# Kernel tuning notes

Hardware: AMD Instinct MI355X
Metric: run time of the kernel (lower is better)

The kernel has to match this reference:

```python
import jax, jax.numpy as jnp
import numpy as np

M, N, D, K = 32, 8192, 64, 16


def setup_inputs() -> dict:
    key = jax.random.key(0)
    ks = jax.random.split(key, 5)
    X = jax.random.normal(ks[0], (N, D), jnp.float32)
    pi = jax.nn.softmax(jax.random.normal(ks[1], (M,), jnp.float32))  # valid mixture weights
    mu = jax.random.normal(ks[2], (M, D), jnp.float32)
    Lambda_j = 0.1 * jax.random.normal(ks[3], (M, D, K), jnp.float32)  # matches .normal_(0, 0.1) init
    Psi = jax.random.uniform(ks[4], (D,), jnp.float32) + 0.1  # positive diagonal noise variances
    return {"X": X, "pi": pi, "mu": mu, "Lambda_j": Lambda_j, "Psi": Psi}


def _e_step(X, pi, mu, Lambda_j, Psi):
    d = X.shape[1]
    k = Lambda_j.shape[2]
    diag_psi = jnp.diag(Psi) + 1e-6 * jnp.eye(d, dtype=X.dtype)
    # Sigma_j = Lambda_j @ Lambda_j^T + diag(Psi), batched over components: [M,D,D]
    Sigma = jnp.einsum('mdk,mek->mde', Lambda_j, Lambda_j) + diag_psi
    chol = jnp.linalg.cholesky(Sigma)  # [M,D,D], same factorization MultivariateNormal uses
    diff = X[None, :, :] - mu[:, None, :]  # [M,N,D]
    # Mahalanobis term via triangular solve: sol = L^{-1} diff^T  -> [M,D,N]
    sol = jax.vmap(lambda L, Dm: jax.scipy.linalg.solve_triangular(L, Dm.T, lower=True))(chol, diff)
    maha = jnp.sum(sol * sol, axis=1)  # [M,N]
    logdet = 2.0 * jnp.sum(jnp.log(jnp.diagonal(chol, axis1=1, axis2=2)), axis=1)  # [M]
    log_prob = -0.5 * (d * jnp.log(2.0 * jnp.pi) + maha) - 0.5 * logdet[:, None]  # [M,N]
    log_h = (jnp.log(pi + 1e-10)[:, None] + log_prob).T  # [N,M]
    responsibilities = jax.nn.softmax(log_h, axis=1)
    # beta_j = Lambda_j^T Sigma_j^{-1}, via Cholesky solve (same math as torch.inverse path)
    SigInvL = jax.vmap(lambda L, Lam: jax.scipy.linalg.cho_solve((L, True), Lam))(chol, Lambda_j)  # [M,D,K]
    beta = jnp.swapaxes(SigInvL, 1, 2)  # [M,K,D]
    e_z = jnp.einsum('mnd,mkd->mnk', diff, beta)  # [M,N,K]
    term1 = jnp.eye(k, dtype=X.dtype) - jnp.einsum('mkd,mdj->mkj', beta, Lambda_j)  # [M,K,K]
    e_zz = term1[:, None, :, :] + jnp.einsum('mni,mnj->mnij', e_z, e_z)  # [M,N,K,K]
    return responsibilities, e_z, e_zz


def reference(X, pi, mu, Lambda_j, Psi):
    return _e_step(X, pi, mu, Lambda_j, Psi)
```

## Files before the change

kernel.cpp:

```cpp
#include <hip/hip_runtime.h>
#include <math.h>

#define MM 32
#define NN 8192
#define DD 64
#define KK 16

__global__ __launch_bounds__(256) void mfa_pre(
    const float* __restrict__ pi, const float* __restrict__ Lambda,
    const float* __restrict__ Psi, float* __restrict__ Minv_out,
    float* __restrict__ const_out) {
  const int m = blockIdx.x;
  const int tid = threadIdx.x;
  __shared__ float lam[DD * KK];
  __shared__ float pinv[DD];
  __shared__ float Mmat[KK * KK];
  __shared__ float Lmat[KK * KK];
  __shared__ float vbuf[KK];

  for (int idx = tid; idx < DD * KK; idx += 256)
    lam[idx] = Lambda[(size_t)m * DD * KK + idx];
  if (tid < DD) pinv[tid] = 1.0f / (Psi[tid] + 1e-6f);
  __syncthreads();

  {
    const int k = tid >> 4, j = tid & 15;
    float a = 0.0f;
    for (int d = 0; d < DD; ++d)
      a += lam[d * KK + k] * lam[d * KK + j] * pinv[d];
    Mmat[tid] = a + (k == j ? 1.0f : 0.0f);
  }
  __syncthreads();

  float lr[KK];
  if (tid < KK) {
#pragma unroll
    for (int j = 0; j < KK; ++j) lr[j] = Mmat[tid * KK + j];
  }
#pragma unroll
  for (int c = 0; c < KK; ++c) {
    if (tid < KK) vbuf[tid] = lr[c];
    __syncthreads();
    if (tid < KK) {
      const float vc = vbuf[c];
      const float dc = sqrtf(vc);
      const float lrc = lr[c] / dc;
      if (tid >= c) Lmat[tid * KK + c] = lrc;
      const float s = lr[c] / vc;
#pragma unroll
      for (int j = 0; j < KK; ++j)
        if (j > c) lr[j] -= s * vbuf[j];
    }
    __syncthreads();
  }

  if (tid < KK) {
    const int col = tid;
    float y[KK], z[KK];
#pragma unroll
    for (int i = 0; i < KK; ++i) {
      float s = (i == col) ? 1.0f : 0.0f;
#pragma unroll
      for (int p = 0; p < KK; ++p)
        if (p < i) s -= Lmat[i * KK + p] * y[p];
      y[i] = s / Lmat[i * KK + i];
    }
#pragma unroll
    for (int i = KK - 1; i >= 0; --i) {
      float s = y[i];
#pragma unroll
      for (int p = 0; p < KK; ++p)
        if (p > i) s -= Lmat[p * KK + i] * z[p];
      z[i] = s / Lmat[i * KK + i];
    }
#pragma unroll
    for (int i = 0; i < KK; ++i)
      Minv_out[(size_t)m * KK * KK + i * KK + col] = z[i];
  }

  if (tid == 0) {
    float logdetM = 0.0f;
#pragma unroll
    for (int c = 0; c < KK; ++c) logdetM += logf(Lmat[c * KK + c]);
    logdetM *= 2.0f;
    float logdetP = 0.0f;
    for (int d = 0; d < DD; ++d) logdetP -= logf(pinv[d]);
    const float LOG2PI = 1.8378770664093453f;
    const_out[m] =
        logf(pi[m] + 1e-10f) - 0.5f * (DD * LOG2PI + logdetP + logdetM);
  }
}

__global__ __launch_bounds__(256) void mfa_main(
    const float* __restrict__ X, const float* __restrict__ mu,
    const float* __restrict__ Lambda, const float* __restrict__ Psi,
    const float* __restrict__ Minv, const float* __restrict__ cconst,
    float* __restrict__ out) {
  const int m = blockIdx.y;
  const int n0 = blockIdx.x * 256;
  const int tid = threadIdx.x;

  __shared__ float Wl[DD * KK];
  __shared__ float pinv[DD];
  __shared__ float mul[DD];
  __shared__ float minv_l[KK * KK];
  __shared__ float ez_l[256 * KK];

  if (tid < DD) {
    pinv[tid] = 1.0f / (Psi[tid] + 1e-6f);
    mul[tid] = mu[m * DD + tid];
  }
  minv_l[tid] = Minv[(size_t)m * KK * KK + tid];
  __syncthreads();
  for (int idx = tid; idx < DD * KK; idx += 256)
    Wl[idx] = Lambda[(size_t)m * DD * KK + idx] * pinv[idx >> 4];
  __syncthreads();

  const int n = n0 + tid;
  const float cst = cconst[m];

  float u[KK];
#pragma unroll
  for (int k = 0; k < KK; ++k) u[k] = 0.0f;
  float q = 0.0f;
  const float4* X4 = reinterpret_cast<const float4*>(X + (size_t)n * DD);
#pragma unroll
  for (int d4 = 0; d4 < DD / 4; ++d4) {
    const float4 xv = X4[d4];
    const float xs[4] = {xv.x, xv.y, xv.z, xv.w};
#pragma unroll
    for (int s = 0; s < 4; ++s) {
      const int d = d4 * 4 + s;
      const float df = xs[s] - mul[d];
      q += df * df * pinv[d];
#pragma unroll
      for (int k = 0; k < KK; ++k) u[k] += Wl[d * KK + k] * df;
    }
  }

  float ez[KK];
  float udot = 0.0f;
#pragma unroll
  for (int i = 0; i < KK; ++i) {
    float s = 0.0f;
#pragma unroll
    for (int j = 0; j < KK; ++j) s += minv_l[i * KK + j] * u[j];
    ez[i] = s;
    udot += u[i] * s;
  }
  const float maha = q - udot;
  out[(size_t)n * MM + m] = cst - 0.5f * maha;

#pragma unroll
  for (int k = 0; k < KK; ++k) ez_l[tid * KK + k] = ez[k];
  __syncthreads();

  const float4* ezl4 = reinterpret_cast<const float4*>(ez_l);
  float4* ezout4 = reinterpret_cast<float4*>(
      out + (size_t)NN * MM + ((size_t)m * NN + n0) * KK);
#pragma unroll
  for (int it = 0; it < 4; ++it) ezout4[it * 256 + tid] = ezl4[it * 256 + tid];

  float4* zzout4 =
      reinterpret_cast<float4*>(out + (size_t)NN * MM + (size_t)MM * NN * KK) +
      ((size_t)m * NN + n0) * (KK * KK / 4);
  const int w = tid >> 6, l = tid & 63;
  const int i_ = l >> 2, jq = l & 3;
  const float4 mreg = reinterpret_cast<const float4*>(minv_l)[l];
  for (int it = 0; it < 64; ++it) {
    const int nl = it * 4 + w;
    const float ezi = ez_l[nl * KK + i_];
    const float4 ezj = ezl4[nl * 4 + jq];
    float4 o;
    o.x = mreg.x + ezi * ezj.x;
    o.y = mreg.y + ezi * ezj.y;
    o.z = mreg.z + ezi * ezj.z;
    o.w = mreg.w + ezi * ezj.w;
    zzout4[(size_t)it * 256 + tid] = o;
  }
}

__global__ __launch_bounds__(256) void mfa_softmax(float* __restrict__ out) {
  const int n = blockIdx.x * 256 + threadIdx.x;
  float4* p = reinterpret_cast<float4*>(out) + (size_t)n * (MM / 4);
  float v[MM];
#pragma unroll
  for (int i = 0; i < MM / 4; ++i) {
    const float4 t = p[i];
    v[4 * i] = t.x; v[4 * i + 1] = t.y; v[4 * i + 2] = t.z; v[4 * i + 3] = t.w;
  }
  float mx = -3.4e38f;
#pragma unroll
  for (int i = 0; i < MM; ++i) mx = fmaxf(mx, v[i]);
  float s = 0.0f;
#pragma unroll
  for (int i = 0; i < MM; ++i) { v[i] = expf(v[i] - mx); s += v[i]; }
  const float inv = 1.0f / s;
#pragma unroll
  for (int i = 0; i < MM / 4; ++i) {
    float4 t;
    t.x = v[4 * i] * inv; t.y = v[4 * i + 1] * inv;
    t.z = v[4 * i + 2] * inv; t.w = v[4 * i + 3] * inv;
    p[i] = t;
  }
}

extern "C" void kernel_launch(void* const* d_in, const int* in_sizes, int n_in,
                              void* d_out, int out_size, void* d_ws,
                              size_t ws_size, hipStream_t stream) {
  const float* X = (const float*)d_in[0];
  const float* pi = (const float*)d_in[1];
  const float* mu = (const float*)d_in[2];
  const float* Lambda = (const float*)d_in[3];
  const float* Psi = (const float*)d_in[4];
  float* out = (float*)d_out;

  float* Minv = (float*)d_ws;
  float* cconst = Minv + MM * KK * KK;

  mfa_pre<<<MM, 256, 0, stream>>>(pi, Lambda, Psi, Minv, cconst);
  mfa_main<<<dim3(NN / 256, MM), 256, 0, stream>>>(X, mu, Lambda, Psi, Minv,
                                                   cconst, out);
  mfa_softmax<<<NN / 256, 256, 0, stream>>>(out);
}
```

Baseline: 80.41 us.

## Split e_zz outer-product writes into separate kernel with nontemporal stores

Moves the large e_zz output generation (M*N*K*K floats) out of the main compute kernel into a dedicated kernel that re-reads e_z from global memory and writes with nontemporal stores across many more, smaller blocks. The intent is to spread the write-bandwidth-bound phase over more blocks and keep the streaming output from polluting the cache. It adds an extra kernel launch and a re-read of e_z from global memory.

After: 103.5 us. 28.7% more time.

```diff
diff --git a/kernel.cpp b/kernel.cpp
--- a/kernel.cpp
+++ b/kernel.cpp
@@ -5,6 +5,8 @@
 #define NN 8192
 #define DD 64
 #define KK 16
+
+typedef float f32x4 __attribute__((ext_vector_type(4)));
 
 __global__ __launch_bounds__(256) void mfa_pre(
     const float* __restrict__ pi, const float* __restrict__ Lambda,
@@ -91,7 +93,7 @@
   }
 }
 
-__global__ __launch_bounds__(256) void mfa_main(
+__global__ __launch_bounds__(256) void mfa_compute(
     const float* __restrict__ X, const float* __restrict__ mu,
     const float* __restrict__ Lambda, const float* __restrict__ Psi,
     const float* __restrict__ Minv, const float* __restrict__ cconst,
@@ -160,23 +162,26 @@
       out + (size_t)NN * MM + ((size_t)m * NN + n0) * KK);
 #pragma unroll
   for (int it = 0; it < 4; ++it) ezout4[it * 256 + tid] = ezl4[it * 256 + tid];
-
-  float4* zzout4 =
-      reinterpret_cast<float4*>(out + (size_t)NN * MM + (size_t)MM * NN * KK) +
-      ((size_t)m * NN + n0) * (KK * KK / 4);
+}
+
+__global__ __launch_bounds__(256) void mfa_ezz(
+    const float* __restrict__ ez, const float* __restrict__ Minv,
+    float* __restrict__ outzz) {
+  const int tid = threadIdx.x;
   const int w = tid >> 6, l = tid & 63;
   const int i_ = l >> 2, jq = l & 3;
-  const float4 mreg = reinterpret_cast<const float4*>(minv_l)[l];
-  for (int it = 0; it < 64; ++it) {
-    const int nl = it * 4 + w;
-    const float ezi = ez_l[nl * KK + i_];
-    const float4 ezj = ezl4[nl * 4 + jq];
-    float4 o;
-    o.x = mreg.x + ezi * ezj.x;
-    o.y = mreg.y + ezi * ezj.y;
-    o.z = mreg.z + ezi * ezj.z;
-    o.w = mreg.w + ezi * ezj.w;
-    zzout4[(size_t)it * 256 + tid] = o;
+  const long long s0 = (long long)blockIdx.x * 128;
+  const int m = (int)(s0 / NN);
+  const f32x4 mreg = reinterpret_cast<const f32x4*>(Minv)[m * 64 + l];
+  const f32x4* ez4 = reinterpret_cast<const f32x4*>(ez);
+  f32x4* out4 = reinterpret_cast<f32x4*>(outzz);
+#pragma unroll 4
+  for (int it = 0; it < 32; ++it) {
+    const long long s = s0 + it * 4 + w;
+    const float ezi = ez[s * KK + i_];
+    const f32x4 ezj = ez4[s * 4 + jq];
+    const f32x4 o = mreg + ezi * ezj;
+    __builtin_nontemporal_store(o, &out4[s * 64 + l]);
   }
 }
 
@@ -218,8 +223,12 @@
   float* Minv = (float*)d_ws;
   float* cconst = Minv + MM * KK * KK;
 
+  float* ez_out = out + (size_t)NN * MM;
+  float* ezz_out = ez_out + (size_t)MM * NN * KK;
+
   mfa_pre<<<MM, 256, 0, stream>>>(pi, Lambda, Psi, Minv, cconst);
-  mfa_main<<<dim3(NN / 256, MM), 256, 0, stream>>>(X, mu, Lambda, Psi, Minv,
-                                                   cconst, out);
+  mfa_compute<<<dim3(NN / 256, MM), 256, 0, stream>>>(X, mu, Lambda, Psi, Minv,
+                                                      cconst, out);
+  mfa_ezz<<<(MM * NN) / 128, 256, 0, stream>>>(ez_out, Minv, ezz_out);
   mfa_softmax<<<NN / 256, 256, 0, stream>>>(out);
 }
```
